# Kernel tuning notes

Hardware: AMD Instinct MI355X
Metric: run time of the kernel (lower is better)

The kernel has to match this reference:

```python
import jax, jax.numpy as jnp
import numpy as np

N = 256        # SSM state size
D_MODEL = 2048 # number of independent channels sharing the kernel
L_MAX = 4096   # sequence length


def setup_inputs() -> dict:
    key = jax.random.key(0)
    k1, k2, k3, k4 = jax.random.split(key, 4)
    s = float(np.sqrt(N))
    # Stable A: eigenvalues with negative real part so A^l stays bounded after
    # bilinear discretization with step = 1/L.
    A = 0.5 * jax.random.normal(k1, (N, N), jnp.float32) / s - jnp.eye(N, dtype=jnp.float32)
    B = jax.random.normal(k2, (N, 1), jnp.float32) / s   # lecun-scale
    C = jax.random.normal(k3, (1, N), jnp.float32) / s
    D = jnp.ones((1,), jnp.float32)
    y = jax.random.normal(k4, (D_MODEL, L_MAX), jnp.float32)
    return {"y": y, "A": A, "B": B, "C": C, "D": D}


def _build_kernel(A, B, C, L, step):
    # Bilinear (Tustin) discretization, as in discretize_SSM.
    I = jnp.eye(A.shape[0], dtype=A.dtype)
    BL = jnp.linalg.inv(I - (step / 2.0) * A)
    Abar = BL @ (I + (step / 2.0) * A)
    Bbar = (BL * step) @ B                      # (N, 1)
    # K[l] = C @ Abar^l @ Bbar, computed as L matvecs via scan
    # (same math as the matrix_power loop, without O(L*N^3) cost).
    def step_fn(x, _):
        return Abar @ x, (C @ x)[0]
    _, K = jax.lax.scan(step_fn, Bbar[:, 0], None, length=L)
    return K                                     # (L,)


def _causal_conv(y, K):
    # mode='full' convolution truncated to first L samples == causal conv.
    L = y.shape[-1]
    n = 2 * L
    Yf = jnp.fft.rfft(y, n=n, axis=-1)           # (d_model, n//2+1)
    Kf = jnp.fft.rfft(K, n=n)                    # (n//2+1,)
    return jnp.fft.irfft(Yf * Kf, n=n, axis=-1)[..., :L]


def reference(y, A, B, C, D):
    L = y.shape[-1]
    K = _build_kernel(A, B, C, L, step=1.0 / L)
    return _causal_conv(y, K) + D * y
```

## Files before the change

kernel.cpp:

```cpp
#include <hip/hip_runtime.h>

#define N_ 256
#define L_ 4096
#define DM_ 2048
#define STEPF (1.0f / 4096.0f)
#define NW 10
#define NV 5
#define RQN 4608

typedef short bf16x8 __attribute__((ext_vector_type(8)));
typedef float f32x4 __attribute__((ext_vector_type(4)));
typedef float f32x16 __attribute__((ext_vector_type(16)));
typedef unsigned int uint32;

__device__ __forceinline__ uint32 bf16rne(float f) {
    uint32 u = __builtin_bit_cast(uint32, f);
    return (u + 0x7FFFu + ((u >> 16) & 1u)) >> 16;
}
__device__ __forceinline__ float rdlane(float v, int l) {
    return __builtin_bit_cast(float, __builtin_amdgcn_readlane(__builtin_bit_cast(int, v), l));
}
__device__ __forceinline__ float hif(float x) {
    return __builtin_bit_cast(float, __builtin_bit_cast(uint32, x) & 0xFFFF0000u);
}
#define PK2(LO, HI) __builtin_amdgcn_perm(__builtin_bit_cast(uint32, (HI)), \
                                          __builtin_bit_cast(uint32, (LO)), 0x07060302u)

__global__ __launch_bounds__(1024) void k_build(const float* __restrict__ Araw,
                                                const float* __restrict__ Bv,
                                                const float* __restrict__ Cv,
                                                const float* __restrict__ yf,
                                                uint2* __restrict__ Rqg,
                                                uint4* __restrict__ ybf) {
    const int tid = threadIdx.x;
    if (blockIdx.x > 0) {
        const size_t base = (size_t)(blockIdx.x - 1) * 32768;
        const float4* yin = (const float4*)(yf + base);
        uint4* yo = ybf + base / 8;
#pragma unroll
        for (int i = 0; i < 4; ++i) {
            int c = i * 1024 + tid;
            float4 q0 = yin[2 * c], q1 = yin[2 * c + 1];
            uint4 o; o.x = PK2(q0.x, q0.y); o.y = PK2(q0.z, q0.w);
                     o.z = PK2(q1.x, q1.y); o.w = PK2(q1.z, q1.w);
            yo[c] = o;
        }
        return;
    }

    __shared__ float sm[39168];
    float* kry = sm;
    float* red = sm + 3840;
    float* Wl  = sm + 5888;
    float* Vt  = sm + 22528;
    float* Kf  = sm;

    const int j = tid & 255, seg = tid >> 8, lane = tid & 63;
    const int e = 64 * seg + lane;
    float a[64];

#define DOT64(S0, S1, VV) { \
    _Pragma("unroll") \
    for (int m = 0; m < 64; m += 2) { \
        S0 = fmaf(rdlane(VV, m), a[m], S0); \
        S1 = fmaf(rdlane(VV, m + 1), a[m + 1], S1); \
    } }

#pragma unroll
    for (int m = 0; m < 64; ++m) a[m] = Araw[(64 * seg + m) * 256 + j];
    if (tid < 256) kry[tid] = Cv[tid];
    __syncthreads();
    const float WSC = 4032.0f / 4096.0f;
    {
        float vv = kry[e];
        for (int n = 1; n < NW; ++n) {
            float s0 = 0.f, s1 = 0.f;
            DOT64(s0, s1, vv)
            float* rb = red + (n & 1) * 1024;
            rb[seg * 256 + j] = s0 + s1;
            __syncthreads();
            float sc = WSC / (float)n;
            vv = (rb[e] + rb[256 + e] + rb[512 + e] + rb[768 + e]) * sc;
            if (tid < 256)
                kry[n * 256 + tid] = (rb[tid] + rb[256 + tid] + rb[512 + tid] + rb[768 + tid]) * sc;
        }
    }
    __syncthreads();
    {
        float kj[NW];
#pragma unroll
        for (int n = 0; n < NW; ++n) kj[n] = kry[n * 256 + j];
#pragma unroll
        for (int u = 0; u < 16; ++u) {
            int q = seg + 4 * u;
            float c = (float)q * (1.0f / 63.0f);
            float h = kj[NW - 1];
#pragma unroll
            for (int n = NW - 2; n >= 0; --n) h = fmaf(c, h, kj[n]);
            Wl[q * 260 + j] = h;
        }
    }
    {
        const float4* Ar = (const float4*)(Araw + (size_t)j * 256 + 64 * seg);
#pragma unroll
        for (int m4 = 0; m4 < 16; ++m4) {
            float4 q4 = Ar[m4];
            a[4 * m4] = q4.x; a[4 * m4 + 1] = q4.y; a[4 * m4 + 2] = q4.z; a[4 * m4 + 3] = q4.w;
        }
    }
    const float ms = 0.5f * STEPF;
    const float bve = Bv[e];
    {
        float vv = bve;
        for (int it = 0; it < 2; ++it) {
            float s0 = 0.f, s1 = 0.f;
            DOT64(s0, s1, vv)
            float* rb = red + (it & 1) * 1024;
            rb[seg * 256 + j] = s0 + s1;
            __syncthreads();
            vv = fmaf(ms, rb[e] + rb[256 + e] + rb[512 + e] + rb[768 + e], bve);
            if (it == 1 && tid < 256) {
                float su = rb[tid] + rb[256 + tid] + rb[512 + tid] + rb[768 + tid];
                kry[tid] = STEPF * fmaf(ms, su, Bv[tid]);
            }
        }
    }
    __syncthreads();
    const float VSC = 63.0f / 4096.0f;
    {
        float vv = kry[e];
        for (int n = 1; n < NV; ++n) {
            float s0 = 0.f, s1 = 0.f;
            DOT64(s0, s1, vv)
            float* rb = red + (n & 1) * 1024;
            rb[seg * 256 + j] = s0 + s1;
            __syncthreads();
            float sc = VSC / (float)n;
            vv = (rb[e] + rb[256 + e] + rb[512 + e] + rb[768 + e]) * sc;
            if (tid < 256)
                kry[n * 256 + tid] = (rb[tid] + rb[256 + tid] + rb[512 + tid] + rb[768 + tid]) * sc;
        }
    }
    __syncthreads();
    {
        float kj[NV];
#pragma unroll
        for (int n = 0; n < NV; ++n) kj[n] = kry[n * 256 + j];
#pragma unroll
        for (int u = 0; u < 16; ++u) {
            int r = seg + 4 * u;
            float c = (float)r * (1.0f / 63.0f);
            float h = kj[NV - 1];
#pragma unroll
            for (int n = NV - 2; n >= 0; --n) h = fmaf(c, h, kj[n]);
            Vt[r * 260 + j] = h;
        }
    }
    __syncthreads();
    {
        const int wv = tid >> 6;
        const int qt = wv >> 2, rt = wv & 3;
        const int n16 = lane & 15, g4 = lane >> 4;
        const int q = 16 * qt + n16;
        const int r = 16 * rt + n16;
        f32x4 ac = (f32x4){0.f, 0.f, 0.f, 0.f};
        for (int s = 0; s < 8; ++s) {
            const int kk = 32 * s + 8 * g4;
            float4 w0 = *(const float4*)&Wl[q * 260 + kk];
            float4 w1 = *(const float4*)&Wl[q * 260 + kk + 4];
            float4 v0 = *(const float4*)&Vt[r * 260 + kk];
            float4 v1 = *(const float4*)&Vt[r * 260 + kk + 4];
            uint4 uh; uh.x = PK2(w0.x, w0.y); uh.y = PK2(w0.z, w0.w);
                      uh.z = PK2(w1.x, w1.y); uh.w = PK2(w1.z, w1.w);
            float l0 = w0.x - hif(w0.x), l1 = w0.y - hif(w0.y);
            float l2 = w0.z - hif(w0.z), l3 = w0.w - hif(w0.w);
            float l4 = w1.x - hif(w1.x), l5 = w1.y - hif(w1.y);
            float l6 = w1.z - hif(w1.z), l7 = w1.w - hif(w1.w);
            uint4 ul; ul.x = PK2(l0, l1); ul.y = PK2(l2, l3);
                      ul.z = PK2(l4, l5); ul.w = PK2(l6, l7);
            uint4 uv; uv.x = PK2(v0.x, v0.y); uv.y = PK2(v0.z, v0.w);
                      uv.z = PK2(v1.x, v1.y); uv.w = PK2(v1.z, v1.w);
            ac = __builtin_amdgcn_mfma_f32_16x16x32_bf16(__builtin_bit_cast(bf16x8, uh),
                                                         __builtin_bit_cast(bf16x8, uv), ac, 0, 0, 0);
            ac = __builtin_amdgcn_mfma_f32_16x16x32_bf16(__builtin_bit_cast(bf16x8, ul),
                                                         __builtin_bit_cast(bf16x8, uv), ac, 0, 0, 0);
        }
#pragma unroll
        for (int jj = 0; jj < 4; ++jj)
            Kf[(16 * qt + 4 * g4 + jj) * 64 + r] = ac[jj];
    }
    __syncthreads();
    for (int i = tid; i < RQN; i += 1024) {
        int aa = 4095 - i;
        uint32 e0 = (aa >= 0) ? bf16rne(Kf[aa]) : 0u;
        uint32 e1 = (aa >= 1) ? bf16rne(Kf[aa - 1]) : 0u;
        uint32 e2 = (aa >= 2) ? bf16rne(Kf[aa - 2]) : 0u;
        uint32 e3 = (aa >= 3) ? bf16rne(Kf[aa - 3]) : 0u;
        uint2 v; v.x = e0 | (e1 << 16); v.y = e2 | (e3 << 16);
        Rqg[i] = v;
    }
#undef DOT64
}

__global__ __launch_bounds__(256, 2) void k_conv(const uint2* __restrict__ Rqg,
                                                 const uint4* __restrict__ ybf,
                                                 const float* __restrict__ y,
                                                 const float* __restrict__ Dp,
                                                 float* __restrict__ out) {
    __shared__ uint2 Rq[RQN];
    __shared__ f32x4 mbuf[2][8][64];
    const int tid = threadIdx.x;
#pragma unroll
    for (int i = 0; i < RQN / 256; ++i) Rq[i * 256 + tid] = Rqg[i * 256 + tid];
    __syncthreads();

    const int w = tid >> 6, lane = tid & 63;
    const int m32 = lane & 31, h = lane >> 5;
    const int ds = w & 1, jh = w >> 1;
    const int by = (int)blockIdx.y;
    const int d0w = (int)blockIdx.x * 64 + ds * 32;
    const int d = d0w + m32;
    const uint4* __restrict__ ybr = ybf + (size_t)d * (L_ / 8);
    const float D0 = Dp[0];

#define LOADF(SL, I0) { \
    uint2 u0 = Rq[(I0)]; uint2 u1 = Rq[(I0) + 4]; \
    uint4 uu; uu.x = u0.x; uu.y = u0.y; uu.z = u1.x; uu.w = u1.y; \
    fr[SL] = __builtin_bit_cast(bf16x8, uu); }
#define MFT(TT, SL) acc[TT] = __builtin_amdgcn_mfma_f32_32x32x16_bf16(fr[SL], bv, acc[TT], 0, 0, 0);

#define STEPE(P) { \
    bv = __builtin_bit_cast(bf16x8, ave); \
    MFT(3, ((P) + 1) & 3) \
    LOADF(((P) + 1) & 3, bcurE) bcurE += 32; \
    ave = ybr[yn & 511]; yn += 2; \
    MFT(0, (P) & 3) MFT(1, ((P) + 3) & 3) MFT(2, ((P) + 2) & 3) \
}
#define STEPO(P) { \
    bv = __builtin_bit_cast(bf16x8, avo); \
    MFT(3, 4 + (((P) + 1) & 3)) \
    LOADF(4 + (((P) + 1) & 3), bcurO) bcurO += 32; \
    avo = ybr[yn & 511]; yn += 2; \
    MFT(0, 4 + ((P) & 3)) MFT(1, 4 + (((P) + 3) & 3)) MFT(2, 4 + (((P) + 2) & 3)) \
}

#define ROUND8() \
    STEPE(0) STEPO(0) STEPE(1) STEPO(1) STEPE(2) STEPO(2) STEPE(3) STEPO(3)
#define REM4() \
    STEPE(0) STEPO(0) STEPE(1) STEPO(1)

    for (int strip = 0; strip < 2; ++strip) {
        const int v = strip ? by : (31 - by);
        const int t0 = v << 7;
        const int Sh = 2 * (v + 1);
        const int ShW = 4 * (v + 1);
        const int s0 = jh * ShW;
        (void)Sh;

        f32x16 acc[4] = {};
        bf16x8 fr[8], bv;
        uint4 ave, avo;

        const int IB = 4095 - t0 - m32 + 8 * h + 16 * s0;
        LOADF(0, IB)      LOADF(3, IB - 32) LOADF(2, IB - 64) LOADF(1, IB - 96)
        LOADF(4, IB + 16) LOADF(7, IB - 16) LOADF(6, IB - 48) LOADF(5, IB - 80)
        ave = ybr[(2 * s0 + h) & 511];
        avo = ybr[(2 * s0 + 2 + h) & 511];
        int bcurE = IB + 32, bcurO = IB + 48;
        int yn = 2 * s0 + 4 + h;

        const int n8 = ShW >> 3;
        for (int it = 0; it < n8; ++it) {
            ROUND8()
        }
        if (ShW & 4) {
            REM4()
        }

#pragma unroll
        for (int rr = 0; rr < 2; ++rr) {
            if (jh == 1) {
#pragma unroll
                for (int tp = 0; tp < 2; ++tp)
#pragma unroll
                    for (int c = 0; c < 4; ++c) {
                        f32x4 ch = {acc[2 * rr + tp][4 * c], acc[2 * rr + tp][4 * c + 1],
                                    acc[2 * rr + tp][4 * c + 2], acc[2 * rr + tp][4 * c + 3]};
                        mbuf[ds][4 * tp + c][lane] = ch;
                    }
            }
            __syncthreads();
            if (jh == 0) {
#pragma unroll
                for (int tp = 0; tp < 2; ++tp)
#pragma unroll
                    for (int c = 0; c < 4; ++c) {
                        f32x4 mm = mbuf[ds][4 * tp + c][lane];
                        acc[2 * rr + tp][4 * c]     += mm[0];
                        acc[2 * rr + tp][4 * c + 1] += mm[1];
                        acc[2 * rr + tp][4 * c + 2] += mm[2];
                        acc[2 * rr + tp][4 * c + 3] += mm[3];
                    }
            }
            __syncthreads();
        }
        if (jh == 0) {
#pragma unroll
            for (int tt = 0; tt < 4; ++tt) {
#pragma unroll
                for (int q = 0; q < 4; ++q) {
                    int tb = t0 + 32 * tt + 8 * q + 4 * h;
                    size_t ix = (size_t)d * L_ + tb;
                    float4 yv = *(const float4*)&y[ix];
                    float4 o;
                    o.x = acc[tt][4 * q]     + D0 * yv.x;
                    o.y = acc[tt][4 * q + 1] + D0 * yv.y;
                    o.z = acc[tt][4 * q + 2] + D0 * yv.z;
                    o.w = acc[tt][4 * q + 3] + D0 * yv.w;
                    *(float4*)&out[ix] = o;
                }
            }
        }
    }

#undef ROUND8
#undef REM4
#undef STEPE
#undef STEPO
#undef MFT
#undef LOADF
}


extern "C" void kernel_launch(void* const* d_in, const int* in_sizes, int n_in,
                              void* d_out, int out_size, void* d_ws, size_t ws_size,
                              hipStream_t stream) {
    const float* y  = (const float*)d_in[0];
    const float* A  = (const float*)d_in[1];
    const float* Bv = (const float*)d_in[2];
    const float* Cv = (const float*)d_in[3];
    const float* Dp = (const float*)d_in[4];
    float* out = (float*)d_out;
    char* w = (char*)d_ws;
    uint2* Rqg = (uint2*)w;
    uint4* ybf = (uint4*)(w + 36864);

    k_build<<<dim3(257), dim3(1024), 0, stream>>>(A, Bv, Cv, y, Rqg, ybf);
    k_conv<<<dim3(32, 16), dim3(256), 0, stream>>>(Rqg, ybf, y, Dp, out);

    (void)in_sizes; (void)n_in; (void)out_size; (void)ws_size;
}
```

Baseline: 80.85 us.

## Switch Toeplitz convolution MFMA from bf16 to fp8 with scaled kernel taps

Quantizes both the input signal and the scaled SSM kernel taps to fp8 (e4m3) instead of bf16. The convolution then uses the 32x32x64 fp8 scaled MFMA, which covers four times the K-depth per instruction, and the loop is restructured to match. The kernel is pre-multiplied by 2^17 and the result rescaled to keep the small taps inside fp8 range. This halves the staging bytes and doubles the matrix throughput per instruction, but it cuts precision sharply and may fail the accuracy tolerance.

```diff
diff --git a/kernel.cpp b/kernel.cpp
--- a/kernel.cpp
+++ b/kernel.cpp
@@ -6,17 +6,16 @@
 #define STEPF (1.0f / 4096.0f)
 #define NW 10
 #define NV 5
-#define RQN 4608
+#define RBN 4608
+#define KSC 131072.0f
+#define KSCI 7.62939453125e-06f
 
 typedef short bf16x8 __attribute__((ext_vector_type(8)));
+typedef int i32x8 __attribute__((ext_vector_type(8)));
 typedef float f32x4 __attribute__((ext_vector_type(4)));
 typedef float f32x16 __attribute__((ext_vector_type(16)));
 typedef unsigned int uint32;
 
-__device__ __forceinline__ uint32 bf16rne(float f) {
-    uint32 u = __builtin_bit_cast(uint32, f);
-    return (u + 0x7FFFu + ((u >> 16) & 1u)) >> 16;
-}
 __device__ __forceinline__ float rdlane(float v, int l) {
     return __builtin_bit_cast(float, __builtin_amdgcn_readlane(__builtin_bit_cast(int, v), l));
 }
@@ -25,26 +24,36 @@
 }
 #define PK2(LO, HI) __builtin_amdgcn_perm(__builtin_bit_cast(uint32, (HI)), \
                                           __builtin_bit_cast(uint32, (LO)), 0x07060302u)
+__device__ __forceinline__ int pk4f8(float a, float b, float c, float d) {
+    int r = __builtin_amdgcn_cvt_pk_fp8_f32(a, b, 0, false);
+    r = __builtin_amdgcn_cvt_pk_fp8_f32(c, d, r, true);
+    return r;
+}
 
 __global__ __launch_bounds__(1024) void k_build(const float* __restrict__ Araw,
                                                 const float* __restrict__ Bv,
                                                 const float* __restrict__ Cv,
                                                 const float* __restrict__ yf,
-                                                uint2* __restrict__ Rqg,
-                                                uint4* __restrict__ ybf) {
+                                                uint2* __restrict__ Rb8g,
+                                                uint4* __restrict__ yf8) {
     const int tid = threadIdx.x;
     if (blockIdx.x > 0) {
-        const size_t base = (size_t)(blockIdx.x - 1) * 32768;
-        const float4* yin = (const float4*)(yf + base);
-        uint4* yo = ybf + base / 8;
-#pragma unroll
-        for (int i = 0; i < 4; ++i) {
-            int c = i * 1024 + tid;
-            float4 q0 = yin[2 * c], q1 = yin[2 * c + 1];
-            uint4 o; o.x = PK2(q0.x, q0.y); o.y = PK2(q0.z, q0.w);
-                     o.z = PK2(q1.x, q1.y); o.w = PK2(q1.z, q1.w);
-            yo[c] = o;
-        }
+        const size_t co = (size_t)(blockIdx.x - 1) * 1024 + tid;
+        const float4* yin = (const float4*)(yf + co * 32);
+        float4 q[8];
+#pragma unroll
+        for (int i = 0; i < 8; ++i) q[i] = yin[i];
+        uint4 o0, o1;
+        o0.x = pk4f8(q[0].x, q[0].y, q[0].z, q[0].w);
+        o0.y = pk4f8(q[1].x, q[1].y, q[1].z, q[1].w);
+        o0.z = pk4f8(q[2].x, q[2].y, q[2].z, q[2].w);
+        o0.w = pk4f8(q[3].x, q[3].y, q[3].z, q[3].w);
+        o1.x = pk4f8(q[4].x, q[4].y, q[4].z, q[4].w);
+        o1.y = pk4f8(q[5].x, q[5].y, q[5].z, q[5].w);
+        o1.z = pk4f8(q[6].x, q[6].y, q[6].z, q[6].w);
+        o1.w = pk4f8(q[7].x, q[7].y, q[7].z, q[7].w);
+        yf8[2 * co] = o0;
+        yf8[2 * co + 1] = o1;
         return;
     }
 
@@ -190,28 +199,32 @@
             Kf[(16 * qt + 4 * g4 + jj) * 64 + r] = ac[jj];
     }
     __syncthreads();
-    for (int i = tid; i < RQN; i += 1024) {
-        int aa = 4095 - i;
-        uint32 e0 = (aa >= 0) ? bf16rne(Kf[aa]) : 0u;
-        uint32 e1 = (aa >= 1) ? bf16rne(Kf[aa - 1]) : 0u;
-        uint32 e2 = (aa >= 2) ? bf16rne(Kf[aa - 2]) : 0u;
-        uint32 e3 = (aa >= 3) ? bf16rne(Kf[aa - 3]) : 0u;
-        uint2 v; v.x = e0 | (e1 << 16); v.y = e2 | (e3 << 16);
-        Rqg[i] = v;
+
+    for (int i = tid; i < RBN; i += 1024) {
+        float v[8];
+#pragma unroll
+        for (int b = 0; b < 8; ++b) {
+            int idx = 4095 - i - b;
+            v[b] = (idx >= 0) ? Kf[idx] * KSC : 0.f;
+        }
+        uint2 o;
+        o.x = (uint32)pk4f8(v[0], v[1], v[2], v[3]);
+        o.y = (uint32)pk4f8(v[4], v[5], v[6], v[7]);
+        Rb8g[i] = o;
     }
 #undef DOT64
 }
 
-__global__ __launch_bounds__(256, 2) void k_conv(const uint2* __restrict__ Rqg,
-                                                 const uint4* __restrict__ ybf,
+__global__ __launch_bounds__(256, 2) void k_conv(const uint2* __restrict__ Rb8g,
+                                                 const uint4* __restrict__ yf8,
                                                  const float* __restrict__ y,
                                                  const float* __restrict__ Dp,
                                                  float* __restrict__ out) {
-    __shared__ uint2 Rq[RQN];
+    __shared__ uint2 Rb8[RBN];
     __shared__ f32x4 mbuf[2][8][64];
     const int tid = threadIdx.x;
 #pragma unroll
-    for (int i = 0; i < RQN / 256; ++i) Rq[i * 256 + tid] = Rqg[i * 256 + tid];
+    for (int i = 0; i < RBN / 256; ++i) Rb8[i * 256 + tid] = Rb8g[i * 256 + tid];
     __syncthreads();
 
     const int w = tid >> 6, lane = tid & 63;
@@ -220,61 +233,62 @@
     const int by = (int)blockIdx.y;
     const int d0w = (int)blockIdx.x * 64 + ds * 32;
     const int d = d0w + m32;
-    const uint4* __restrict__ ybr = ybf + (size_t)d * (L_ / 8);
+    const uint4* __restrict__ yq8 = yf8 + (size_t)d * (L_ / 16);
     const float D0 = Dp[0];
 
-#define LOADF(SL, I0) { \
-    uint2 u0 = Rq[(I0)]; uint2 u1 = Rq[(I0) + 4]; \
-    uint4 uu; uu.x = u0.x; uu.y = u0.y; uu.z = u1.x; uu.w = u1.y; \
-    fr[SL] = __builtin_bit_cast(bf16x8, uu); }
-#define MFT(TT, SL) acc[TT] = __builtin_amdgcn_mfma_f32_32x32x16_bf16(fr[SL], bv, acc[TT], 0, 0, 0);
-
-#define STEPE(P) { \
-    bv = __builtin_bit_cast(bf16x8, ave); \
-    MFT(3, ((P) + 1) & 3) \
-    LOADF(((P) + 1) & 3, bcurE) bcurE += 32; \
-    ave = ybr[yn & 511]; yn += 2; \
-    MFT(0, (P) & 3) MFT(1, ((P) + 3) & 3) MFT(2, ((P) + 2) & 3) \
-}
-#define STEPO(P) { \
-    bv = __builtin_bit_cast(bf16x8, avo); \
-    MFT(3, 4 + (((P) + 1) & 3)) \
-    LOADF(4 + (((P) + 1) & 3), bcurO) bcurO += 32; \
-    avo = ybr[yn & 511]; yn += 2; \
-    MFT(0, 4 + ((P) & 3)) MFT(1, 4 + (((P) + 3) & 3)) MFT(2, 4 + (((P) + 2) & 3)) \
-}
-
-#define ROUND8() \
-    STEPE(0) STEPO(0) STEPE(1) STEPO(1) STEPE(2) STEPO(2) STEPE(3) STEPO(3)
-#define REM4() \
-    STEPE(0) STEPO(0) STEPE(1) STEPO(1)
+#define LOADF8(SL, E) { \
+    uint2 q0 = Rb8[(E)]; uint2 q1 = Rb8[(E) + 8]; uint2 q2 = Rb8[(E) + 16]; uint2 q3 = Rb8[(E) + 24]; \
+    i32x8 f; f[0] = (int)q0.x; f[1] = (int)q0.y; f[2] = (int)q1.x; f[3] = (int)q1.y; \
+    f[4] = (int)q2.x; f[5] = (int)q2.y; f[6] = (int)q3.x; f[7] = (int)q3.y; \
+    fr[SL] = f; }
+#define MKB(BA, BB) { \
+    i32x8 f; f[0] = (int)(BA).x; f[1] = (int)(BA).y; f[2] = (int)(BA).z; f[3] = (int)(BA).w; \
+    f[4] = (int)(BB).x; f[5] = (int)(BB).y; f[6] = (int)(BB).z; f[7] = (int)(BB).w; \
+    bv = f; }
+#define MFT(TT, SL) acc[TT] = __builtin_amdgcn_mfma_scale_f32_32x32x64_f8f6f4( \
+    fr[SL], bv, acc[TT], 0, 0, 0, 0x7F7F7F7F, 0, 0x7F7F7F7F);
+
+#define STEPE() { \
+    MKB(avea, aveb); \
+    MFT(2, 2) MFT(3, 3) \
+    LOADF8(2, bcur + 64) LOADF8(3, bcur + 32) \
+    avea = yq8[yn & 255]; aveb = yq8[(yn + 1) & 255]; \
+    yn += 4; bcur += 64; \
+    MFT(0, 0) MFT(1, 1) \
+}
+#define STEPO() { \
+    MKB(avoa, avob); \
+    MFT(2, 0) MFT(3, 1) \
+    LOADF8(0, bcur + 64) LOADF8(1, bcur + 32) \
+    avoa = yq8[yn & 255]; avob = yq8[(yn + 1) & 255]; \
+    yn += 4; bcur += 64; \
+    MFT(0, 2) MFT(1, 3) \
+}
 
     for (int strip = 0; strip < 2; ++strip) {
         const int v = strip ? by : (31 - by);
         const int t0 = v << 7;
-        const int Sh = 2 * (v + 1);
-        const int ShW = 4 * (v + 1);
+        const int ShW = v + 1;
         const int s0 = jh * ShW;
-        (void)Sh;
 
         f32x16 acc[4] = {};
-        bf16x8 fr[8], bv;
-        uint4 ave, avo;
-
-        const int IB = 4095 - t0 - m32 + 8 * h + 16 * s0;
-        LOADF(0, IB)      LOADF(3, IB - 32) LOADF(2, IB - 64) LOADF(1, IB - 96)
-        LOADF(4, IB + 16) LOADF(7, IB - 16) LOADF(6, IB - 48) LOADF(5, IB - 80)
-        ave = ybr[(2 * s0 + h) & 511];
-        avo = ybr[(2 * s0 + 2 + h) & 511];
-        int bcurE = IB + 32, bcurO = IB + 48;
-        int yn = 2 * s0 + 4 + h;
-
-        const int n8 = ShW >> 3;
-        for (int it = 0; it < n8; ++it) {
-            ROUND8()
-        }
-        if (ShW & 4) {
-            REM4()
+        i32x8 fr[4], bv;
+        uint4 avea, aveb, avoa, avob;
+
+        const int B0 = 4095 - t0 - m32 + 32 * h + 64 * s0;
+        LOADF8(0, B0) LOADF8(1, B0 - 32) LOADF8(2, B0 - 64) LOADF8(3, B0 - 96)
+        avea = yq8[(4 * s0 + 2 * h) & 255];     aveb = yq8[(4 * s0 + 2 * h + 1) & 255];
+        avoa = yq8[(4 * s0 + 4 + 2 * h) & 255]; avob = yq8[(4 * s0 + 5 + 2 * h) & 255];
+        int bcur = B0;
+        int yn = 4 * s0 + 8 + 2 * h;
+
+        const int nr = ShW >> 1;
+        for (int it = 0; it < nr; ++it) {
+            STEPE()
+            STEPO()
+        }
+        if (ShW & 1) {
+            STEPE()
         }
 
 #pragma unroll
@@ -313,22 +327,21 @@
                     size_t ix = (size_t)d * L_ + tb;
                     float4 yv = *(const float4*)&y[ix];
                     float4 o;
-                    o.x = acc[tt][4 * q]     + D0 * yv.x;
-                    o.y = acc[tt][4 * q + 1] + D0 * yv.y;
-                    o.z = acc[tt][4 * q + 2] + D0 * yv.z;
-                    o.w = acc[tt][4 * q + 3] + D0 * yv.w;
+                    o.x = acc[tt][4 * q]     * KSCI + D0 * yv.x;
+                    o.y = acc[tt][4 * q + 1] * KSCI + D0 * yv.y;
+                    o.z = acc[tt][4 * q + 2] * KSCI + D0 * yv.z;
+                    o.w = acc[tt][4 * q + 3] * KSCI + D0 * yv.w;
                     *(float4*)&out[ix] = o;
                 }
             }
         }
     }
 
-#undef ROUND8
-#undef REM4
 #undef STEPE
 #undef STEPO
 #undef MFT
-#undef LOADF
+#undef MKB
+#undef LOADF8
 }
 
 
@@ -342,11 +355,11 @@
     const float* Dp = (const float*)d_in[4];
     float* out = (float*)d_out;
     char* w = (char*)d_ws;
-    uint2* Rqg = (uint2*)w;
-    uint4* ybf = (uint4*)(w + 36864);
-
-    k_build<<<dim3(257), dim3(1024), 0, stream>>>(A, Bv, Cv, y, Rqg, ybf);
-    k_conv<<<dim3(32, 16), dim3(256), 0, stream>>>(Rqg, ybf, y, Dp, out);
+    uint2* Rb8g = (uint2*)w;
+    uint4* yf8  = (uint4*)(w + 36864);
+
+    k_build<<<dim3(257), dim3(1024), 0, stream>>>(A, Bv, Cv, y, Rb8g, yf8);
+    k_conv<<<dim3(32, 16), dim3(256), 0, stream>>>(Rb8g, yf8, y, Dp, out);
 
     (void)in_sizes; (void)n_in; (void)out_size; (void)ws_size;
 }
```

Result: faster. 64.76 us (-19.9%).
